# Performance work log

Measured on AMD Instinct MI355X. Metric: run time of the kernel, lower is better.

Reference implementation:

```python
import jax, jax.numpy as jnp
import numpy as np

N_HEADS = 16
HEAD_SIZE = 64
EMBED = 1024
BLOCK = 2048
B, T = 2, 2048


def setup_inputs() -> dict:
    key = jax.random.key(0)
    ks = jax.random.split(key, 6)
    scale = 0.02
    inputs = jax.random.normal(ks[0], (B, T, EMBED), dtype=jnp.float32)
    # per-head projection weights, stacked: [H, E, D]
    Wk = jax.random.normal(ks[1], (N_HEADS, EMBED, HEAD_SIZE), dtype=jnp.float32) * scale
    Wq = jax.random.normal(ks[2], (N_HEADS, EMBED, HEAD_SIZE), dtype=jnp.float32) * scale
    Wv = jax.random.normal(ks[3], (N_HEADS, EMBED, HEAD_SIZE), dtype=jnp.float32) * scale
    Wo = jax.random.normal(ks[4], (EMBED, EMBED), dtype=jnp.float32) * scale
    bo = jax.random.normal(ks[5], (EMBED,), dtype=jnp.float32) * scale
    return {"inputs": inputs, "Wk": Wk, "Wq": Wq, "Wv": Wv, "Wo": Wo, "bo": bo}


def reference(inputs, Wk, Wq, Wv, Wo, bo):
    # per-head projections: [B,H,T,D]
    k = jnp.einsum("bte,hed->bhtd", inputs, Wk)
    q = jnp.einsum("bte,hed->bhtd", inputs, Wq)
    v = jnp.einsum("bte,hed->bhtd", inputs, Wv)
    # NOTE: original computes wei = K @ Q^T (faithful reproduction)
    wei = jnp.einsum("bhtd,bhsd->bhts", k, q) * (HEAD_SIZE ** -0.5)
    causal = jnp.tril(jnp.ones((T, T), dtype=bool))  # tril==0 masked
    wei = jnp.where(causal, wei, -jnp.inf)
    wei = jax.nn.softmax(wei, axis=-1)
    out = jnp.einsum("bhts,bhsd->bhtd", wei, v)
    # concat heads along feature dim: [B,T,H*D]
    z = out.transpose(0, 2, 1, 3).reshape(B, T, N_HEADS * HEAD_SIZE)
    z = z @ Wo.T + bo  # match torch Linear(x) = x @ W^T + b
    return z
```

## Files before the change

### kernel.cpp

```cpp
#include <hip/hip_runtime.h>
#include <cstdint>
#include <cstddef>

typedef __bf16 bf8_t __attribute__((ext_vector_type(8)));
typedef float  f4_t  __attribute__((ext_vector_type(4)));

static __device__ __forceinline__ f4_t mfma16(bf8_t a, bf8_t b, f4_t c) {
    return __builtin_amdgcn_mfma_f32_16x16x32_bf16(a, b, c, 0, 0, 0);
}

#if defined(__has_builtin) && __has_builtin(__builtin_amdgcn_exp2f)
#define EXP2F(x) __builtin_amdgcn_exp2f(x)
#else
#define EXP2F(x) exp2f(x)
#endif

static __device__ __forceinline__ void async_ld16(const __bf16* g, __bf16* l) {
    __builtin_amdgcn_global_load_lds(
        (const __attribute__((address_space(1))) void*)(uintptr_t)g,
        (__attribute__((address_space(3))) void*)(uintptr_t)l, 16, 0, 0);
}


__global__ void __launch_bounds__(256) prep_convert(const float* __restrict__ X,
                                                    const float* __restrict__ Wo,
                                                    __bf16* __restrict__ Xbf,
                                                    __bf16* __restrict__ Wobf) {
    size_t bx = blockIdx.x;
    const float* src; __bf16* dst; size_t base;
    if (bx < 2048) { src = X;  dst = Xbf;  base = bx * 2048; }
    else           { src = Wo; dst = Wobf; base = (bx - 2048) * 2048; }
    size_t i = base + (size_t)threadIdx.x * 8;
    float4 a = *(const float4*)(src + i);
    float4 b = *(const float4*)(src + i + 4);
    bf8_t o;
    o[0] = (__bf16)a.x; o[1] = (__bf16)a.y; o[2] = (__bf16)a.z; o[3] = (__bf16)a.w;
    o[4] = (__bf16)b.x; o[5] = (__bf16)b.y; o[6] = (__bf16)b.z; o[7] = (__bf16)b.w;
    *(bf8_t*)(dst + i) = o;
}

__global__ void __launch_bounds__(256) wtrans(const float* __restrict__ Wq,
                                              const float* __restrict__ Wk,
                                              const float* __restrict__ Wv,
                                              __bf16* __restrict__ Wqt,
                                              __bf16* __restrict__ Wkt,
                                              __bf16* __restrict__ Wvt) {
    const float* W; __bf16* Wt;
    if (blockIdx.y == 0)      { W = Wq; Wt = Wqt; }
    else if (blockIdx.y == 1) { W = Wk; Wt = Wkt; }
    else                      { W = Wv; Wt = Wvt; }
    int h = blockIdx.x >> 4, eb = blockIdx.x & 15;
    __shared__ float tile[64][65];
    int tx = threadIdx.x;
    int e = tx >> 2, dg = (tx & 3) * 16;
    const float* src = W + ((size_t)h * 1024 + eb * 64 + e) * 64 + dg;
#pragma unroll
    for (int i = 0; i < 4; ++i) {
        float4 v = *(const float4*)(src + i * 4);
        tile[dg + i * 4 + 0][e] = v.x;
        tile[dg + i * 4 + 1][e] = v.y;
        tile[dg + i * 4 + 2][e] = v.z;
        tile[dg + i * 4 + 3][e] = v.w;
    }
    __syncthreads();
    int d = tx >> 2, eg = (tx & 3) * 16;
    __bf16* dst = Wt + (size_t)(h * 64 + d) * 1024 + eb * 64 + eg;
    bf8_t o0, o1;
#pragma unroll
    for (int i = 0; i < 8; ++i) o0[i] = (__bf16)tile[d][eg + i];
#pragma unroll
    for (int i = 0; i < 8; ++i) o1[i] = (__bf16)tile[d][eg + 8 + i];
    *(bf8_t*)dst       = o0;
    *(bf8_t*)(dst + 8) = o1;
}

static __device__ __forceinline__ void gemm_tile(const __bf16* __restrict__ A,
                                                 const __bf16* __restrict__ Bt,
                                                 __bf16* As, __bf16* Bs,
                                                 int m0, int n0, f4_t acc[4][2]) {
    const int tid  = threadIdx.x;
    const int lane = tid & 63;
    const int wv   = tid >> 6;
    const int lrow = lane >> 3;
    const int lsc  = lane & 7;
    const int quad = lane >> 4;
    const int l15  = lane & 15;
    const int wm = (wv & 1) * 64;
    const int wn = (wv >> 1) * 32;
    f4_t zero = {0.f, 0.f, 0.f, 0.f};
#pragma unroll
    for (int mi = 0; mi < 4; ++mi)
#pragma unroll
        for (int ni = 0; ni < 2; ++ni) acc[mi][ni] = zero;

    for (int kb = 0; kb < 16; ++kb) {
#pragma unroll
        for (int j = 0; j < 4; ++j) {
            int row = wv * 32 + j * 8 + lrow;
            int lc  = lsc ^ (row & 7);
            async_ld16(A + (size_t)(m0 + row) * 1024 + kb * 64 + lc * 8,
                       As + (wv * 32 + j * 8) * 64);
        }
#pragma unroll
        for (int j = 0; j < 2; ++j) {
            int row = wv * 16 + j * 8 + lrow;
            int lc  = lsc ^ (row & 7);
            async_ld16(Bt + (size_t)(n0 + row) * 1024 + kb * 64 + lc * 8,
                       Bs + (wv * 16 + j * 8) * 64);
        }
        __syncthreads();
#pragma unroll
        for (int ks = 0; ks < 2; ++ks) {
            bf8_t af[4], bfr[2];
#pragma unroll
            for (int mi = 0; mi < 4; ++mi) {
                int row = wm + mi * 16 + l15;
                int ch  = (ks * 4 + quad) ^ (row & 7);
                af[mi] = *(const bf8_t*)(As + row * 64 + ch * 8);
            }
#pragma unroll
            for (int ni = 0; ni < 2; ++ni) {
                int row = wn + ni * 16 + l15;
                int ch  = (ks * 4 + quad) ^ (row & 7);
                bfr[ni] = *(const bf8_t*)(Bs + row * 64 + ch * 8);
            }
#pragma unroll
            for (int mi = 0; mi < 4; ++mi)
#pragma unroll
                for (int ni = 0; ni < 2; ++ni)
                    acc[mi][ni] = mfma16(af[mi], bfr[ni], acc[mi][ni]);
        }
        __syncthreads();
    }
}

__global__ void __launch_bounds__(256) gemm_proj(const __bf16* __restrict__ Xbf,
                                                 const __bf16* __restrict__ Wqt,
                                                 const __bf16* __restrict__ Wkt,
                                                 const __bf16* __restrict__ Wvt,
                                                 __bf16* __restrict__ Qb,
                                                 __bf16* __restrict__ Kb,
                                                 __bf16* __restrict__ Vt) {
    __shared__ __bf16 smem[128 * 64 + 64 * 64];
    __bf16* As = smem;
    __bf16* Bs = smem + 128 * 64;
    int which = blockIdx.y;
    const __bf16* Bt = which == 0 ? Wqt : (which == 1 ? Wkt : Wvt);
    int m0 = ((int)blockIdx.x >> 4) * 128;
    int n0 = ((int)blockIdx.x & 15) * 64;
    f4_t acc[4][2];
    gemm_tile(Xbf, Bt, As, Bs, m0, n0, acc);
    const int lane = threadIdx.x & 63, wv = threadIdx.x >> 6;
    const int quad = lane >> 4, l15 = lane & 15;
    const int wm = (wv & 1) * 64, wn = (wv >> 1) * 32;
    if (which < 2) {
        __bf16* C = which ? Kb : Qb;
        const float scl = which ? 0.18033688f : 1.0f;
#pragma unroll
        for (int mi = 0; mi < 4; ++mi)
#pragma unroll
            for (int ni = 0; ni < 2; ++ni)
#pragma unroll
                for (int r = 0; r < 4; ++r) {
                    int m = m0 + wm + mi * 16 + quad * 4 + r;
                    int n = n0 + wn + ni * 16 + l15;
                    int b = m >> 11, t = m & 2047;
                    int h = n >> 6,  d = n & 63;
                    C[((size_t)(b * 16 + h) * 2048 + t) * 64 + d] = (__bf16)(acc[mi][ni][r] * scl);
                }
    } else {
        const int STR = 136;
#pragma unroll
        for (int mi = 0; mi < 4; ++mi)
#pragma unroll
            for (int ni = 0; ni < 2; ++ni)
#pragma unroll
                for (int r = 0; r < 4; ++r) {
                    int tl = wm + mi * 16 + quad * 4 + r;
                    int dl = wn + ni * 16 + l15;
                    smem[dl * STR + tl] = (__bf16)acc[mi][ni][r];
                }
        __syncthreads();
        int b = m0 >> 11, h = n0 >> 6, tg0 = m0 & 2047;
        int d  = (int)threadIdx.x >> 2;
        int tc = ((int)threadIdx.x & 3) * 32;
        __bf16* dst = Vt + ((size_t)(b * 16 + h) * 64 + d) * 2048 + tg0 + tc;
        const __bf16* srcl = smem + d * STR + tc;
#pragma unroll
        for (int k = 0; k < 4; ++k)
            *(bf8_t*)(dst + k * 8) = *(const bf8_t*)(srcl + k * 8);
    }
}

__global__ void __launch_bounds__(256) gemm_out(const __bf16* __restrict__ Ob,
                                                const __bf16* __restrict__ Wobf,
                                                const float* __restrict__ bo,
                                                float* __restrict__ out) {
    __shared__ __bf16 smem[128 * 64 + 64 * 64];
    __bf16* As = smem;
    __bf16* Bs = smem + 128 * 64;
    int m0 = ((int)blockIdx.x >> 4) * 128;
    int n0 = ((int)blockIdx.x & 15) * 64;
    f4_t acc[4][2];
    gemm_tile(Ob, Wobf, As, Bs, m0, n0, acc);
    const int lane = threadIdx.x & 63, wv = threadIdx.x >> 6;
    const int quad = lane >> 4, l15 = lane & 15;
    const int wm = (wv & 1) * 64, wn = (wv >> 1) * 32;
#pragma unroll
    for (int mi = 0; mi < 4; ++mi)
#pragma unroll
        for (int ni = 0; ni < 2; ++ni)
#pragma unroll
            for (int r = 0; r < 4; ++r) {
                int m = m0 + wm + mi * 16 + quad * 4 + r;
                int n = n0 + wn + ni * 16 + l15;
                out[(size_t)m * 1024 + n] = acc[mi][ni][r] + bo[n];
            }
}

__global__ void __launch_bounds__(256, 4) attn(const __bf16* __restrict__ Kb,
                                               const __bf16* __restrict__ Qb,
                                               const __bf16* __restrict__ Vt,
                                               __bf16* __restrict__ Ob,
                                               int* __restrict__ ctrs) {
    __shared__ __bf16 Qs[64 * 64];
    __shared__ __bf16 Vs[64 * 64];
    __shared__ __bf16 Ps[4][16 * 72];
    __shared__ int item_lds;
    const int tid = threadIdx.x, lane = tid & 63, wv = tid >> 6;
    const int quad = lane >> 4, l15 = lane & 15;
    const int lrow8 = lane >> 3, lchunk = lane & 7;
    int xcc;
    asm volatile("s_getreg_b32 %0, hwreg(HW_REG_XCC_ID)" : "=s"(xcc));
    xcc &= 7;
    int* ctr = ctrs + xcc * 16;
    __bf16* Psw = &Ps[wv][0];
    f4_t zero = {0.f, 0.f, 0.f, 0.f};

    for (;;) {
        if (tid == 0) item_lds = atomicAdd(ctr, 1);
        __syncthreads();
        const int q = item_lds;
        if (q >= 128) break;
        const int tt = 31 - (q >> 2);
        const int bh = xcc * 4 + (q & 3);
        const int b = bh >> 4, h = bh & 15;
        const int t0 = tt * 64;
        const int tw = t0 + wv * 16;
        const __bf16* Kp = Kb + (size_t)bh * 2048 * 64;
        const __bf16* Qp = Qb + (size_t)bh * 2048 * 64;
        const __bf16* Vp = Vt + (size_t)bh * 64 * 2048;

        bf8_t kfrag[2];
#pragma unroll
        for (int ks = 0; ks < 2; ++ks)
            kfrag[ks] = *(const bf8_t*)(Kp + (size_t)(tw + l15) * 64 + ks * 32 + quad * 8);

        f4_t oacc[4];
#pragma unroll
        for (int ni = 0; ni < 4; ++ni) oacc[ni] = zero;
        float lsum[4] = {0.f, 0.f, 0.f, 0.f};

        const int nsb = tt + 1;
        for (int sb = 0; sb < nsb; ++sb) {
            const int s0 = sb * 64;
            const bool masked = (sb == nsb - 1);
#pragma unroll
            for (int j = 0; j < 2; ++j) {
                int row = wv * 8 + j * 32 + lrow8;
                int cg  = lchunk ^ (row & 7);
                async_ld16(Qp + (size_t)(s0 + row) * 64 + cg * 8,
                           Qs + wv * 512 + j * 2048);
            }
#pragma unroll
            for (int j = 0; j < 2; ++j) {
                int row = wv * 8 + j * 32 + lrow8;
                int cg  = lchunk ^ (row & 7);
                async_ld16(Vp + (size_t)row * 2048 + s0 + cg * 8,
                           Vs + wv * 512 + j * 2048);
            }
            __syncthreads();
            f4_t sacc[4] = {zero, zero, zero, zero};
#pragma unroll
            for (int ks = 0; ks < 2; ++ks) {
                bf8_t qf[4];
#pragma unroll
                for (int st = 0; st < 4; ++st) {
                    int row = st * 16 + l15;
                    int ch  = (ks * 4 + quad) ^ (row & 7);
                    qf[st] = *(const bf8_t*)(Qs + row * 64 + ch * 8);
                }
#pragma unroll
                for (int st = 0; st < 4; ++st)
                    sacc[st] = mfma16(kfrag[ks], qf[st], sacc[st]);
            }
#pragma unroll
            for (int st = 0; st < 4; ++st)
#pragma unroll
                for (int r = 0; r < 4; ++r) {
                    float e = EXP2F(sacc[st][r]);
                    if (masked && (s0 + st * 16 + l15 > tw + quad * 4 + r)) e = 0.0f;
                    lsum[r] += e;
                    Psw[(quad * 4 + r) * 72 + st * 16 + l15] = (__bf16)e;
                }
            asm volatile("s_waitcnt lgkmcnt(0)" ::: "memory");
            bf8_t pf[2];
#pragma unroll
            for (int ks = 0; ks < 2; ++ks)
                pf[ks] = *(const bf8_t*)(Psw + l15 * 72 + ks * 32 + quad * 8);
#pragma unroll
            for (int ks = 0; ks < 2; ++ks) {
                bf8_t vf[4];
#pragma unroll
                for (int ni = 0; ni < 4; ++ni) {
                    int row = ni * 16 + l15;
                    int ch  = (ks * 4 + quad) ^ (row & 7);
                    vf[ni] = *(const bf8_t*)(Vs + row * 64 + ch * 8);
                }
#pragma unroll
                for (int ni = 0; ni < 4; ++ni)
                    oacc[ni] = mfma16(pf[ks], vf[ni], oacc[ni]);
            }
            __syncthreads();
        }

#pragma unroll
        for (int r = 0; r < 4; ++r) {
            float l = lsum[r];
            l += __shfl_xor(l, 1);
            l += __shfl_xor(l, 2);
            l += __shfl_xor(l, 4);
            l += __shfl_xor(l, 8);
            float inv = 1.0f / l;
            int t = tw + quad * 4 + r;
#pragma unroll
            for (int ni = 0; ni < 4; ++ni)
                Ob[((size_t)(b * 2048 + t) * 16 + h) * 64 + ni * 16 + l15] =
                    (__bf16)(oacc[ni][r] * inv);
        }
        __syncthreads();
    }
}

extern "C" void kernel_launch(void* const* d_in, const int* in_sizes, int n_in,
                              void* d_out, int out_size, void* d_ws, size_t ws_size,
                              hipStream_t stream) {
    const float* X  = (const float*)d_in[0];
    const float* Wk = (const float*)d_in[1];
    const float* Wq = (const float*)d_in[2];
    const float* Wv = (const float*)d_in[3];
    const float* Wo = (const float*)d_in[4];
    const float* bo = (const float*)d_in[5];
    float* out = (float*)d_out;

    __bf16* ws   = (__bf16*)d_ws;
    __bf16* Xbf  = ws;
    __bf16* Wqt  = ws + 4194304;
    __bf16* Wkt  = ws + 5242880;
    __bf16* Wvt  = ws + 6291456;
    __bf16* Wobf = ws + 7340032;
    __bf16* Qb   = ws + 8388608;
    __bf16* Kb   = ws + 12582912;
    __bf16* Vt   = ws + 16777216;
    __bf16* Ob   = ws + 20971520;
    int* ctrs = (int*)d_ws;

    prep_convert<<<2560, 256, 0, stream>>>(X, Wo, Xbf, Wobf);
    wtrans<<<dim3(256, 3), 256, 0, stream>>>(Wq, Wk, Wv, Wqt, Wkt, Wvt);
    gemm_proj<<<dim3(512, 3), 256, 0, stream>>>(Xbf, Wqt, Wkt, Wvt, Qb, Kb, Vt);
    hipMemsetAsync(ctrs, 0, 512, stream);
    attn<<<1024, 256, 0, stream>>>(Kb, Qb, Vt, Ob, ctrs);
    gemm_out<<<512, 256, 0, stream>>>(Ob, Wobf, bo, out);
}
```

Baseline: 179.7 us.

## Double-buffer attention Q/V tiles and enlarge projection GEMM tiles to 128x128

The attention kernel now double-buffers its Q and V LDS tiles, prefetching the next 64-key block while the current one is computed. This drops one barrier per iteration and the trailing per-item barrier. The occupancy hint falls from 4 to 2 blocks per CU and the persistent grid shrinks to 512. Separately, the QKV projection GEMM moves to 128x128 output tiles with 16 accumulators per wave, giving more reuse per loaded tile at the cost of fewer blocks and more registers.

Measured after the change: 189.3 us. +5.3%, slower.

```diff
diff --git a/kernel.cpp b/kernel.cpp
--- a/kernel.cpp
+++ b/kernel.cpp
@@ -74,6 +74,120 @@
     *(bf8_t*)(dst + 8) = o1;
 }
 
+static __device__ __forceinline__ void gemm_tile128(const __bf16* __restrict__ A,
+                                                    const __bf16* __restrict__ Bt,
+                                                    __bf16* As, __bf16* Bs,
+                                                    int m0, int n0, f4_t acc[4][4]) {
+    const int tid  = threadIdx.x;
+    const int lane = tid & 63;
+    const int wv   = tid >> 6;
+    const int lrow = lane >> 3;
+    const int lsc  = lane & 7;
+    const int quad = lane >> 4;
+    const int l15  = lane & 15;
+    const int wm = (wv & 1) * 64;
+    const int wn = (wv >> 1) * 64;
+    f4_t zero = {0.f, 0.f, 0.f, 0.f};
+#pragma unroll
+    for (int mi = 0; mi < 4; ++mi)
+#pragma unroll
+        for (int ni = 0; ni < 4; ++ni) acc[mi][ni] = zero;
+
+    for (int kb = 0; kb < 16; ++kb) {
+#pragma unroll
+        for (int j = 0; j < 4; ++j) {
+            int row = wv * 32 + j * 8 + lrow;
+            int lc  = lsc ^ (row & 7);
+            async_ld16(A + (size_t)(m0 + row) * 1024 + kb * 64 + lc * 8,
+                       As + (wv * 32 + j * 8) * 64);
+            async_ld16(Bt + (size_t)(n0 + row) * 1024 + kb * 64 + lc * 8,
+                       Bs + (wv * 32 + j * 8) * 64);
+        }
+        __syncthreads();
+#pragma unroll
+        for (int ks = 0; ks < 2; ++ks) {
+            bf8_t af[4], bfr[4];
+#pragma unroll
+            for (int mi = 0; mi < 4; ++mi) {
+                int row = wm + mi * 16 + l15;
+                int ch  = (ks * 4 + quad) ^ (row & 7);
+                af[mi] = *(const bf8_t*)(As + row * 64 + ch * 8);
+            }
+#pragma unroll
+            for (int ni = 0; ni < 4; ++ni) {
+                int row = wn + ni * 16 + l15;
+                int ch  = (ks * 4 + quad) ^ (row & 7);
+                bfr[ni] = *(const bf8_t*)(Bs + row * 64 + ch * 8);
+            }
+#pragma unroll
+            for (int mi = 0; mi < 4; ++mi)
+#pragma unroll
+                for (int ni = 0; ni < 4; ++ni)
+                    acc[mi][ni] = mfma16(af[mi], bfr[ni], acc[mi][ni]);
+        }
+        __syncthreads();
+    }
+}
+
+__global__ void __launch_bounds__(256) gemm_proj(const __bf16* __restrict__ Xbf,
+                                                 const __bf16* __restrict__ Wqt,
+                                                 const __bf16* __restrict__ Wkt,
+                                                 const __bf16* __restrict__ Wvt,
+                                                 __bf16* __restrict__ Qb,
+                                                 __bf16* __restrict__ Kb,
+                                                 __bf16* __restrict__ Vt) {
+    __shared__ __bf16 smem[17408];
+    __bf16* As = smem;
+    __bf16* Bs = smem + 8192;
+    int which = blockIdx.y;
+    const __bf16* Bt = which == 0 ? Wqt : (which == 1 ? Wkt : Wvt);
+    int m0 = ((int)blockIdx.x >> 3) * 128;
+    int n0 = ((int)blockIdx.x & 7) * 128;
+    f4_t acc[4][4];
+    gemm_tile128(Xbf, Bt, As, Bs, m0, n0, acc);
+    const int lane = threadIdx.x & 63, wv = threadIdx.x >> 6;
+    const int quad = lane >> 4, l15 = lane & 15;
+    const int wm = (wv & 1) * 64, wn = (wv >> 1) * 64;
+    if (which < 2) {
+        __bf16* C = which ? Kb : Qb;
+        const float scl = which ? 0.18033688f : 1.0f;
+#pragma unroll
+        for (int mi = 0; mi < 4; ++mi)
+#pragma unroll
+            for (int ni = 0; ni < 4; ++ni)
+#pragma unroll
+                for (int r = 0; r < 4; ++r) {
+                    int m = m0 + wm + mi * 16 + quad * 4 + r;
+                    int n = n0 + wn + ni * 16 + l15;
+                    int b = m >> 11, t = m & 2047;
+                    int h = n >> 6,  d = n & 63;
+                    C[((size_t)(b * 16 + h) * 2048 + t) * 64 + d] = (__bf16)(acc[mi][ni][r] * scl);
+                }
+    } else {
+        const int STR = 136;
+#pragma unroll
+        for (int mi = 0; mi < 4; ++mi)
+#pragma unroll
+            for (int ni = 0; ni < 4; ++ni)
+#pragma unroll
+                for (int r = 0; r < 4; ++r) {
+                    int ml = wm + mi * 16 + quad * 4 + r;
+                    int nl = wn + ni * 16 + l15;
+                    smem[nl * STR + ml] = (__bf16)acc[mi][ni][r];
+                }
+        __syncthreads();
+        int b = m0 >> 11, tg0 = m0 & 2047;
+        int nl = (int)threadIdx.x >> 1;
+        int tc = ((int)threadIdx.x & 1) * 64;
+        int n = n0 + nl, h = n >> 6, d = n & 63;
+        __bf16* dst = Vt + ((size_t)(b * 16 + h) * 64 + d) * 2048 + tg0 + tc;
+        const __bf16* srcl = smem + nl * STR + tc;
+#pragma unroll
+        for (int k = 0; k < 8; ++k)
+            *(bf8_t*)(dst + k * 8) = *(const bf8_t*)(srcl + k * 8);
+    }
+}
+
 static __device__ __forceinline__ void gemm_tile(const __bf16* __restrict__ A,
                                                  const __bf16* __restrict__ Bt,
                                                  __bf16* As, __bf16* Bs,
@@ -134,64 +248,6 @@
     }
 }
 
-__global__ void __launch_bounds__(256) gemm_proj(const __bf16* __restrict__ Xbf,
-                                                 const __bf16* __restrict__ Wqt,
-                                                 const __bf16* __restrict__ Wkt,
-                                                 const __bf16* __restrict__ Wvt,
-                                                 __bf16* __restrict__ Qb,
-                                                 __bf16* __restrict__ Kb,
-                                                 __bf16* __restrict__ Vt) {
-    __shared__ __bf16 smem[128 * 64 + 64 * 64];
-    __bf16* As = smem;
-    __bf16* Bs = smem + 128 * 64;
-    int which = blockIdx.y;
-    const __bf16* Bt = which == 0 ? Wqt : (which == 1 ? Wkt : Wvt);
-    int m0 = ((int)blockIdx.x >> 4) * 128;
-    int n0 = ((int)blockIdx.x & 15) * 64;
-    f4_t acc[4][2];
-    gemm_tile(Xbf, Bt, As, Bs, m0, n0, acc);
-    const int lane = threadIdx.x & 63, wv = threadIdx.x >> 6;
-    const int quad = lane >> 4, l15 = lane & 15;
-    const int wm = (wv & 1) * 64, wn = (wv >> 1) * 32;
-    if (which < 2) {
-        __bf16* C = which ? Kb : Qb;
-        const float scl = which ? 0.18033688f : 1.0f;
-#pragma unroll
-        for (int mi = 0; mi < 4; ++mi)
-#pragma unroll
-            for (int ni = 0; ni < 2; ++ni)
-#pragma unroll
-                for (int r = 0; r < 4; ++r) {
-                    int m = m0 + wm + mi * 16 + quad * 4 + r;
-                    int n = n0 + wn + ni * 16 + l15;
-                    int b = m >> 11, t = m & 2047;
-                    int h = n >> 6,  d = n & 63;
-                    C[((size_t)(b * 16 + h) * 2048 + t) * 64 + d] = (__bf16)(acc[mi][ni][r] * scl);
-                }
-    } else {
-        const int STR = 136;
-#pragma unroll
-        for (int mi = 0; mi < 4; ++mi)
-#pragma unroll
-            for (int ni = 0; ni < 2; ++ni)
-#pragma unroll
-                for (int r = 0; r < 4; ++r) {
-                    int tl = wm + mi * 16 + quad * 4 + r;
-                    int dl = wn + ni * 16 + l15;
-                    smem[dl * STR + tl] = (__bf16)acc[mi][ni][r];
-                }
-        __syncthreads();
-        int b = m0 >> 11, h = n0 >> 6, tg0 = m0 & 2047;
-        int d  = (int)threadIdx.x >> 2;
-        int tc = ((int)threadIdx.x & 3) * 32;
-        __bf16* dst = Vt + ((size_t)(b * 16 + h) * 64 + d) * 2048 + tg0 + tc;
-        const __bf16* srcl = smem + d * STR + tc;
-#pragma unroll
-        for (int k = 0; k < 4; ++k)
-            *(bf8_t*)(dst + k * 8) = *(const bf8_t*)(srcl + k * 8);
-    }
-}
-
 __global__ void __launch_bounds__(256) gemm_out(const __bf16* __restrict__ Ob,
                                                 const __bf16* __restrict__ Wobf,
                                                 const float* __restrict__ bo,
@@ -218,13 +274,13 @@
             }
 }
 
-__global__ void __launch_bounds__(256, 4) attn(const __bf16* __restrict__ Kb,
+__global__ void __launch_bounds__(256, 2) attn(const __bf16* __restrict__ Kb,
                                                const __bf16* __restrict__ Qb,
                                                const __bf16* __restrict__ Vt,
                                                __bf16* __restrict__ Ob,
                                                int* __restrict__ ctrs) {
-    __shared__ __bf16 Qs[64 * 64];
-    __shared__ __bf16 Vs[64 * 64];
+    __shared__ __bf16 Qs[2][64 * 64];
+    __shared__ __bf16 Vs[2][64 * 64];
     __shared__ __bf16 Ps[4][16 * 72];
     __shared__ int item_lds;
     const int tid = threadIdx.x, lane = tid & 63, wv = tid >> 6;
@@ -261,25 +317,28 @@
         for (int ni = 0; ni < 4; ++ni) oacc[ni] = zero;
         float lsum[4] = {0.f, 0.f, 0.f, 0.f};
 
-        const int nsb = tt + 1;
-        for (int sb = 0; sb < nsb; ++sb) {
-            const int s0 = sb * 64;
-            const bool masked = (sb == nsb - 1);
+        auto stage = [&](int buf, int s0) {
 #pragma unroll
             for (int j = 0; j < 2; ++j) {
                 int row = wv * 8 + j * 32 + lrow8;
                 int cg  = lchunk ^ (row & 7);
                 async_ld16(Qp + (size_t)(s0 + row) * 64 + cg * 8,
-                           Qs + wv * 512 + j * 2048);
-            }
-#pragma unroll
-            for (int j = 0; j < 2; ++j) {
-                int row = wv * 8 + j * 32 + lrow8;
-                int cg  = lchunk ^ (row & 7);
+                           &Qs[buf][(wv * 8 + j * 32) * 64]);
                 async_ld16(Vp + (size_t)row * 2048 + s0 + cg * 8,
-                           Vs + wv * 512 + j * 2048);
-            }
+                           &Vs[buf][(wv * 8 + j * 32) * 64]);
+            }
+        };
+
+        const int nsb = tt + 1;
+        stage(0, 0);
+        for (int sb = 0; sb < nsb; ++sb) {
+            const int cur = sb & 1;
+            const int s0 = sb * 64;
+            const bool masked = (sb == nsb - 1);
             __syncthreads();
+            if (sb + 1 < nsb) stage(1 ^ cur, s0 + 64);
+            const __bf16* Qc = &Qs[cur][0];
+            const __bf16* Vc = &Vs[cur][0];
             f4_t sacc[4] = {zero, zero, zero, zero};
 #pragma unroll
             for (int ks = 0; ks < 2; ++ks) {
@@ -288,7 +347,7 @@
                 for (int st = 0; st < 4; ++st) {
                     int row = st * 16 + l15;
                     int ch  = (ks * 4 + quad) ^ (row & 7);
-                    qf[st] = *(const bf8_t*)(Qs + row * 64 + ch * 8);
+                    qf[st] = *(const bf8_t*)(Qc + row * 64 + ch * 8);
                 }
 #pragma unroll
                 for (int st = 0; st < 4; ++st)
@@ -315,13 +374,12 @@
                 for (int ni = 0; ni < 4; ++ni) {
                     int row = ni * 16 + l15;
                     int ch  = (ks * 4 + quad) ^ (row & 7);
-                    vf[ni] = *(const bf8_t*)(Vs + row * 64 + ch * 8);
+                    vf[ni] = *(const bf8_t*)(Vc + row * 64 + ch * 8);
                 }
 #pragma unroll
                 for (int ni = 0; ni < 4; ++ni)
                     oacc[ni] = mfma16(pf[ks], vf[ni], oacc[ni]);
             }
-            __syncthreads();
         }
 
 #pragma unroll
@@ -338,7 +396,6 @@
                 Ob[((size_t)(b * 2048 + t) * 16 + h) * 64 + ni * 16 + l15] =
                     (__bf16)(oacc[ni][r] * inv);
         }
-        __syncthreads();
     }
 }
 
@@ -367,8 +424,8 @@
 
     prep_convert<<<2560, 256, 0, stream>>>(X, Wo, Xbf, Wobf);
     wtrans<<<dim3(256, 3), 256, 0, stream>>>(Wq, Wk, Wv, Wqt, Wkt, Wvt);
-    gemm_proj<<<dim3(512, 3), 256, 0, stream>>>(Xbf, Wqt, Wkt, Wvt, Qb, Kb, Vt);
+    gemm_proj<<<dim3(256, 3), 256, 0, stream>>>(Xbf, Wqt, Wkt, Wvt, Qb, Kb, Vt);
     hipMemsetAsync(ctrs, 0, 512, stream);
-    attn<<<1024, 256, 0, stream>>>(Kb, Qb, Vt, Ob, ctrs);
+    attn<<<512, 256, 0, stream>>>(Kb, Qb, Vt, Ob, ctrs);
     gemm_out<<<512, 256, 0, stream>>>(Ob, Wobf, bo, out);
 }
```
